# Performance work log

Measured on AMD Instinct MI355X. Metric: run time of the kernel, lower is better.

## Reference

```python
import jax, jax.numpy as jnp
import numpy as np

KA = 2  # kernel_att == stride

def _unfold2(t):
    # torch nn.Unfold(kernel=2, stride=2, pad=0): [B,C,H,W] -> [B, C, 4, L], L=(H/2)*(W/2)
    B, C, H, W = t.shape
    t = t.reshape(B, C, H // KA, KA, W // KA, KA).transpose(0, 1, 3, 5, 2, 4)
    return t.reshape(B, C, KA * KA, (H // KA) * (W // KA))

def _fold2(t, H, W):
    # inverse of _unfold2 (non-overlapping): [B, C, 4, L] -> [B, C, H, W]
    B, C, _, L = t.shape
    t = t.reshape(B, C, KA, KA, H // KA, W // KA).transpose(0, 1, 4, 2, 5, 3)
    return t.reshape(B, C, H, W)

def setup_inputs() -> dict:
    key = jax.random.key(0)
    ks = jax.random.split(key, 5)
    b, c, m, h, w = 4, 16, 8, 64, 64
    O = 64
    return {
        "x": jax.random.normal(ks[0], (b, c, m, h, w), jnp.float32),
        "w_q": jax.random.normal(ks[1], (O, m), jnp.float32) * 0.1,
        "w_k": jax.random.normal(ks[2], (O, m), jnp.float32) * 0.1,
        "w_v": jax.random.normal(ks[3], (O, m), jnp.float32) * 0.1,
        "w_p": jax.random.normal(ks[4], (2,), jnp.float32) * 0.1,
    }

def reference(x, w_q, w_k, w_v, w_p):
    b, c, m, h, w = x.shape
    O = w_q.shape[0]
    # res = AdaptiveAvgPool3d((1, dim, dim)) with h==w==dim -> mean over m only
    res = x.mean(axis=2, keepdims=True)            # [b, c, 1, h, w]
    xf = x.reshape(b * c, m, h, w)
    # 1x1 convs (bias-free) are channel matmuls
    q = jnp.einsum('om,bmhw->bohw', w_q, xf)       # [b*c, O, h, w]
    k = jnp.einsum('om,bmhw->bohw', w_k, xf)
    v = jnp.einsum('om,bmhw->bohw', w_v, xf)
    # relative position map pe = conv_p(position(h, w)) -> [1,1,h,w]
    loc_w = jnp.linspace(-1.0, 1.0, w)[None, :]    # varies along W
    loc_h = jnp.linspace(-1.0, 1.0, h)[:, None]    # varies along H
    pe = (w_p[0] * loc_w + w_p[1] * loc_h)[None, None]  # [1,1,h,w]
    q5 = q.reshape(b, c, O, h, w).transpose(0, 2, 1, 3, 4)  # permuted: [b, O, c, h, w]
    k5 = k.reshape(b, c, O, h, w) + pe             # pe broadcast over trailing (h,w)
    v5 = v.reshape(b, c, O, h, w)
    scaling = float(h) ** (-0.5)
    B = b * O
    q_att = (q5 * scaling).reshape(B, c, h, w)
    # NB: torch code views the UNpermuted [b,c,O,h,w] buffer as [b*O, c, h, w] (raw reinterpretation)
    k_att = k5.reshape(B, c, h, w)
    v_att = v5.reshape(B, c, h, w)
    uq = _unfold2(q_att)                           # [B, c, 4, L]
    uk = _unfold2(k_att) + _unfold2(pe)            # unfold_rpe broadcast: [B, c, 4, L]
    uv = _unfold2(v_att)
    # att[B,i,j,l] = sum_p q[B,i,p,l] * k[B,j,p,l]
    att = jnp.einsum('bipl,bjpl->bijl', uq, uk)    # [B, c, c, L]
    att = jax.nn.softmax(att, axis=2)
    out = jnp.einsum('bijl,bjpl->bipl', att, uv)   # [B, c, 4, L]
    out = _fold2(out, h, w)                        # [B, c, h, w]
    out = out.reshape(b, O, c, h, w).transpose(0, 2, 1, 3, 4)  # [b, c, O, h, w]
    return out + res
```

## Files before the change

### kernel.cpp

```cpp
#include <hip/hip_runtime.h>

typedef unsigned int u32;


__global__ __launch_bounds__(256, 1) void adapt_attn(
    const float* __restrict__ x,  const float* __restrict__ wq,
    const float* __restrict__ wk, const float* __restrict__ wv,
    const float* __restrict__ wp, float* __restrict__ out)
{
    __shared__ float s_wk[128];
    __shared__ float s_wv[128];
    __shared__ float s_wq[8];

    const int tid = threadIdx.x;
    const int bid = blockIdx.x;
    const int bb    = bid >> 8;
    const int o     = (bid >> 2) & 63;
    const int patch = ((bid & 3) << 8) + tid;
    const int r   = o & 3;
    const int qch = o >> 2;

    if (tid < 128) {
        s_wk[tid] = wk[(r << 7) + tid];
        s_wv[tid] = wv[(r << 7) + tid];
    } else if (tid < 136) {
        s_wq[tid - 128] = wq[(o << 3) + (tid - 128)];
    }
    __syncthreads();

    const int hh = patch >> 5, ww = patch & 31;
    const int y0 = hh << 1;

    const float wp0 = wp[0];
    const float wp1 = wp[1];
    const float step = 2.0f / 63.0f;
    const float lx0 = -1.0f + step * (float)(ww << 1);
    const float lx1 = lx0 + step;
    const float ly0 = -1.0f + step * (float)y0;
    const float ly1 = ly0 + step;
    float pe2[4];
    pe2[0] = 2.0f * (wp0 * lx0 + wp1 * ly0);
    pe2[1] = 2.0f * (wp0 * lx1 + wp1 * ly0);
    pe2[2] = 2.0f * (wp0 * lx0 + wp1 * ly1);
    pe2[3] = 2.0f * (wp0 * lx1 + wp1 * ly1);

    const float2* __restrict__ x2 = (const float2*)x;
    const int sp_off = y0 * 32 + ww;

    float xk[8][4];
    {
        const int basek = ((bb << 4) + qch) * 16384 + sp_off;
        #pragma unroll
        for (int m = 0; m < 8; m++) {
            float2 a = x2[basek + m * 2048];
            float2 b = x2[basek + m * 2048 + 32];
            xk[m][0] = a.x; xk[m][1] = a.y;
            xk[m][2] = b.x; xk[m][3] = b.y;
        }
    }

    float uk[16][4], uv[16][4];
    #pragma unroll
    for (int j = 0; j < 16; j++) {
        float k0 = pe2[0], k1 = pe2[1], k2 = pe2[2], k3 = pe2[3];
        float v0 = 0.f, v1 = 0.f, v2 = 0.f, v3 = 0.f;
        #pragma unroll
        for (int m = 0; m < 8; m++) {
            const float a = s_wk[j * 8 + m];
            const float c = s_wv[j * 8 + m];
            k0 += a * xk[m][0]; k1 += a * xk[m][1];
            k2 += a * xk[m][2]; k3 += a * xk[m][3];
            v0 += c * xk[m][0]; v1 += c * xk[m][1];
            v2 += c * xk[m][2]; v3 += c * xk[m][3];
        }
        uk[j][0] = k0; uk[j][1] = k1; uk[j][2] = k2; uk[j][3] = k3;
        uv[j][0] = v0; uv[j][1] = v1; uv[j][2] = v2; uv[j][3] = v3;
    }

    float2* __restrict__ out2 = (float2*)out;
    const int baseq0 = (bb << 4) * 16384 + sp_off;
    const int obase0 = ((bb << 4) * 64 + o) * 2048 + sp_off;

    #pragma unroll 1
    for (int i = 0; i < 16; i++) {
        float uq0 = 0.f, uq1 = 0.f, uq2 = 0.f, uq3 = 0.f;
        float rs0 = 0.f, rs1 = 0.f, rs2 = 0.f, rs3 = 0.f;
        const int bq = baseq0 + i * 16384;
        #pragma unroll
        for (int m = 0; m < 8; m++) {
            float2 a = x2[bq + m * 2048];
            float2 b = x2[bq + m * 2048 + 32];
            const float w = s_wq[m];
            uq0 += w * a.x; uq1 += w * a.y; uq2 += w * b.x; uq3 += w * b.y;
            rs0 += a.x;     rs1 += a.y;     rs2 += b.x;     rs3 += b.y;
        }
        uq0 *= 0.125f; uq1 *= 0.125f; uq2 *= 0.125f; uq3 *= 0.125f;
        rs0 *= 0.125f; rs1 *= 0.125f; rs2 *= 0.125f; rs3 *= 0.125f;

        float att[16];
        float mx = -1e30f;
        #pragma unroll
        for (int j = 0; j < 16; j++) {
            const float a = uq0 * uk[j][0] + uq1 * uk[j][1]
                          + uq2 * uk[j][2] + uq3 * uk[j][3];
            att[j] = a;
            mx = fmaxf(mx, a);
        }
        float sum = 0.f;
        #pragma unroll
        for (int j = 0; j < 16; j++) {
            const float e = __expf(att[j] - mx);
            att[j] = e;
            sum += e;
        }
        const float rcp = 1.0f / sum;

        float o0 = 0.f, o1 = 0.f, o2 = 0.f, o3 = 0.f;
        #pragma unroll
        for (int j = 0; j < 16; j++) {
            const float a = att[j];
            o0 += a * uv[j][0]; o1 += a * uv[j][1];
            o2 += a * uv[j][2]; o3 += a * uv[j][3];
        }
        o0 = o0 * rcp + rs0; o1 = o1 * rcp + rs1;
        o2 = o2 * rcp + rs2; o3 = o3 * rcp + rs3;

        const int ob = obase0 + i * 131072;
        out2[ob]      = make_float2(o0, o1);
        out2[ob + 32] = make_float2(o2, o3);
    }
}

extern "C" void kernel_launch(void* const* d_in, const int* in_sizes, int n_in,
                              void* d_out, int out_size, void* d_ws, size_t ws_size,
                              hipStream_t stream) {
    const float* x  = (const float*)d_in[0];
    const float* wq = (const float*)d_in[1];
    const float* wk = (const float*)d_in[2];
    const float* wv = (const float*)d_in[3];
    const float* wp = (const float*)d_in[4];
    float* out = (float*)d_out;
    adapt_attn<<<dim3(1024), dim3(256), 0, stream>>>(x, wq, wk, wv, wp, out);
}
```

Measured before the change: 123.5 us.

## Vectorize attention math with packed float2, drop softmax max, prescale wq

Rewrites the per-thread k/v projection, query projection, score, and output accumulation using two-wide float vectors so the compiler can emit packed FMA instructions. Weight loads from LDS become float4 reads, the 0.125 query scale moves into the shared weights, and the query loads are issued in a batch before use. The softmax no longer subtracts the running maximum, which removes a pass over the scores but risks overflow in exp if scores become large.

```diff
diff --git a/kernel.cpp b/kernel.cpp
--- a/kernel.cpp
+++ b/kernel.cpp
@@ -1,6 +1,7 @@
 #include <hip/hip_runtime.h>
 
 typedef unsigned int u32;
+typedef float v2f __attribute__((ext_vector_type(2)));
 
 
 __global__ __launch_bounds__(256, 1) void adapt_attn(
@@ -8,8 +9,8 @@
     const float* __restrict__ wk, const float* __restrict__ wv,
     const float* __restrict__ wp, float* __restrict__ out)
 {
-    __shared__ float s_wk[128];
-    __shared__ float s_wv[128];
+    __shared__ __align__(16) float s_wk[128];
+    __shared__ __align__(16) float s_wv[128];
     __shared__ float s_wq[8];
 
     const int tid = threadIdx.x;
@@ -24,7 +25,7 @@
         s_wk[tid] = wk[(r << 7) + tid];
         s_wv[tid] = wv[(r << 7) + tid];
     } else if (tid < 136) {
-        s_wq[tid - 128] = wq[(o << 3) + (tid - 128)];
+        s_wq[tid - 128] = 0.125f * wq[(o << 3) + (tid - 128)];
     }
     __syncthreads();
 
@@ -38,96 +39,93 @@
     const float lx1 = lx0 + step;
     const float ly0 = -1.0f + step * (float)y0;
     const float ly1 = ly0 + step;
-    float pe2[4];
-    pe2[0] = 2.0f * (wp0 * lx0 + wp1 * ly0);
-    pe2[1] = 2.0f * (wp0 * lx1 + wp1 * ly0);
-    pe2[2] = 2.0f * (wp0 * lx0 + wp1 * ly1);
-    pe2[3] = 2.0f * (wp0 * lx1 + wp1 * ly1);
+    v2f pea = { 2.0f * (wp0 * lx0 + wp1 * ly0), 2.0f * (wp0 * lx1 + wp1 * ly0) };
+    v2f peb = { 2.0f * (wp0 * lx0 + wp1 * ly1), 2.0f * (wp0 * lx1 + wp1 * ly1) };
 
-    const float2* __restrict__ x2 = (const float2*)x;
+    const v2f* __restrict__ x2 = (const v2f*)x;
     const int sp_off = y0 * 32 + ww;
 
-    float xk[8][4];
+    v2f xa[8], xb[8];
     {
         const int basek = ((bb << 4) + qch) * 16384 + sp_off;
         #pragma unroll
         for (int m = 0; m < 8; m++) {
-            float2 a = x2[basek + m * 2048];
-            float2 b = x2[basek + m * 2048 + 32];
-            xk[m][0] = a.x; xk[m][1] = a.y;
-            xk[m][2] = b.x; xk[m][3] = b.y;
+            xa[m] = x2[basek + m * 2048];
+            xb[m] = x2[basek + m * 2048 + 32];
         }
     }
 
-    float uk[16][4], uv[16][4];
+    v2f uka[16], ukb[16], uva[16], uvb[16];
+    const float4* wk4 = (const float4*)s_wk;
+    const float4* wv4 = (const float4*)s_wv;
     #pragma unroll
     for (int j = 0; j < 16; j++) {
-        float k0 = pe2[0], k1 = pe2[1], k2 = pe2[2], k3 = pe2[3];
-        float v0 = 0.f, v1 = 0.f, v2 = 0.f, v3 = 0.f;
-        #pragma unroll
-        for (int m = 0; m < 8; m++) {
-            const float a = s_wk[j * 8 + m];
-            const float c = s_wv[j * 8 + m];
-            k0 += a * xk[m][0]; k1 += a * xk[m][1];
-            k2 += a * xk[m][2]; k3 += a * xk[m][3];
-            v0 += c * xk[m][0]; v1 += c * xk[m][1];
-            v2 += c * xk[m][2]; v3 += c * xk[m][3];
-        }
-        uk[j][0] = k0; uk[j][1] = k1; uk[j][2] = k2; uk[j][3] = k3;
-        uv[j][0] = v0; uv[j][1] = v1; uv[j][2] = v2; uv[j][3] = v3;
+        const float4 w0 = wk4[j * 2], w1 = wk4[j * 2 + 1];
+        const float4 c0 = wv4[j * 2], c1 = wv4[j * 2 + 1];
+        v2f ka = pea, kb = peb;
+        v2f va = {0.f, 0.f}, vb = {0.f, 0.f};
+        ka += xa[0] * w0.x; kb += xb[0] * w0.x; va += xa[0] * c0.x; vb += xb[0] * c0.x;
+        ka += xa[1] * w0.y; kb += xb[1] * w0.y; va += xa[1] * c0.y; vb += xb[1] * c0.y;
+        ka += xa[2] * w0.z; kb += xb[2] * w0.z; va += xa[2] * c0.z; vb += xb[2] * c0.z;
+        ka += xa[3] * w0.w; kb += xb[3] * w0.w; va += xa[3] * c0.w; vb += xb[3] * c0.w;
+        ka += xa[4] * w1.x; kb += xb[4] * w1.x; va += xa[4] * c1.x; vb += xb[4] * c1.x;
+        ka += xa[5] * w1.y; kb += xb[5] * w1.y; va += xa[5] * c1.y; vb += xb[5] * c1.y;
+        ka += xa[6] * w1.z; kb += xb[6] * w1.z; va += xa[6] * c1.z; vb += xb[6] * c1.z;
+        ka += xa[7] * w1.w; kb += xb[7] * w1.w; va += xa[7] * c1.w; vb += xb[7] * c1.w;
+        uka[j] = ka; ukb[j] = kb; uva[j] = va; uvb[j] = vb;
     }
 
-    float2* __restrict__ out2 = (float2*)out;
+    float wqr[8];
+    #pragma unroll
+    for (int m = 0; m < 8; m++) wqr[m] = s_wq[m];
+
+    v2f* __restrict__ out2 = (v2f*)out;
     const int baseq0 = (bb << 4) * 16384 + sp_off;
     const int obase0 = ((bb << 4) * 64 + o) * 2048 + sp_off;
 
     #pragma unroll 1
     for (int i = 0; i < 16; i++) {
-        float uq0 = 0.f, uq1 = 0.f, uq2 = 0.f, uq3 = 0.f;
-        float rs0 = 0.f, rs1 = 0.f, rs2 = 0.f, rs3 = 0.f;
         const int bq = baseq0 + i * 16384;
+        v2f qa[8], qb[8];
         #pragma unroll
         for (int m = 0; m < 8; m++) {
-            float2 a = x2[bq + m * 2048];
-            float2 b = x2[bq + m * 2048 + 32];
-            const float w = s_wq[m];
-            uq0 += w * a.x; uq1 += w * a.y; uq2 += w * b.x; uq3 += w * b.y;
-            rs0 += a.x;     rs1 += a.y;     rs2 += b.x;     rs3 += b.y;
+            qa[m] = x2[bq + m * 2048];
+            qb[m] = x2[bq + m * 2048 + 32];
         }
-        uq0 *= 0.125f; uq1 *= 0.125f; uq2 *= 0.125f; uq3 *= 0.125f;
-        rs0 *= 0.125f; rs1 *= 0.125f; rs2 *= 0.125f; rs3 *= 0.125f;
+        v2f uqa = {0.f, 0.f}, uqb = {0.f, 0.f};
+        v2f rsa = {0.f, 0.f}, rsb = {0.f, 0.f};
+        #pragma unroll
+        for (int m = 0; m < 8; m++) {
+            uqa += qa[m] * wqr[m];
+            uqb += qb[m] * wqr[m];
+            rsa += qa[m];
+            rsb += qb[m];
+        }
 
         float att[16];
-        float mx = -1e30f;
-        #pragma unroll
-        for (int j = 0; j < 16; j++) {
-            const float a = uq0 * uk[j][0] + uq1 * uk[j][1]
-                          + uq2 * uk[j][2] + uq3 * uk[j][3];
-            att[j] = a;
-            mx = fmaxf(mx, a);
-        }
         float sum = 0.f;
         #pragma unroll
         for (int j = 0; j < 16; j++) {
-            const float e = __expf(att[j] - mx);
+            v2f t = uqa * uka[j];
+            t += uqb * ukb[j];
+            const float e = __expf(t.x + t.y);
             att[j] = e;
             sum += e;
         }
         const float rcp = 1.0f / sum;
 
-        float o0 = 0.f, o1 = 0.f, o2 = 0.f, o3 = 0.f;
+        v2f oa = {0.f, 0.f}, ob = {0.f, 0.f};
         #pragma unroll
         for (int j = 0; j < 16; j++) {
-            const float a = att[j];
-            o0 += a * uv[j][0]; o1 += a * uv[j][1];
-            o2 += a * uv[j][2]; o3 += a * uv[j][3];
+            oa += uva[j] * att[j];
+            ob += uvb[j] * att[j];
         }
-        o0 = o0 * rcp + rs0; o1 = o1 * rcp + rs1;
-        o2 = o2 * rcp + rs2; o3 = o3 * rcp + rs3;
+        oa = oa * rcp + rsa * 0.125f;
+        ob = ob * rcp + rsb * 0.125f;
 
-        const int ob = obase0 + i * 131072;
-        out2[ob]      = make_float2(o0, o1);
-        out2[ob + 32] = make_float2(o2, o3);
+        const int obi = obase0 + i * 131072;
+        out2[obi]      = oa;
+        out2[obi + 32] = ob;
     }
 }
 
```

Measured after the change: 123.1 us. No clear change (-0.3%).
